# Performance work log

Hardware: AMD Instinct MI355X
Metric: run time of the kernel (lower is better)

## Reference

```python
import jax, jax.numpy as jnp
import numpy as np

K = 3          # k_neighbors
EPS = 1e-12    # F.normalize eps


def _l2norm(x):
    n = jnp.sqrt(jnp.sum(x * x, axis=-1, keepdims=True))
    return x / jnp.maximum(n, EPS)


def setup_inputs() -> dict:
    key = jax.random.key(0)
    k1, k2 = jax.random.split(key)
    query_features = jax.random.normal(k1, (64, 64, 32, 32), dtype=jnp.float32)
    support_features = jax.random.normal(k2, (64, 5, 64, 1024), dtype=jnp.float32)
    return {"query_features": query_features, "support_features": support_features}


def reference(query_features, support_features):
    B, D, h, w = query_features.shape
    # (B, Nq, D), L2-normalized along D
    q_local = _l2norm(query_features.reshape(B, D, h * w).transpose(0, 2, 1))
    # support: (B, Way, D, Ns) -> (B, Way, Ns, D), L2-normalized along D
    s_local = _l2norm(support_features.transpose(0, 1, 3, 2))
    # cosine similarities for all (batch, way) pairs in one batched matmul
    sim = jnp.einsum('bqd,bwsd->bwqs', q_local, s_local)  # (B, Way, Nq, Ns)
    k_actual = min(K, sim.shape[-1])
    topk_sim, _ = jax.lax.top_k(sim, k_actual)            # (B, Way, Nq, k)
    return topk_sim.sum(axis=(-1, -2))                    # (B, Way)
```

## Files before the change

kernel.cpp:

```cpp
#include <hip/hip_runtime.h>
#include <hip/hip_bf16.h>


using bf16x8 = __attribute__((ext_vector_type(8))) short;
using f32x4  = __attribute__((ext_vector_type(4))) float;

__device__ inline unsigned cvt_pk_bf16(float lo, float hi) {
    unsigned r;
    asm("v_cvt_pk_bf16_f32 %0, %1, %2" : "=v"(r) : "v"(lo), "v"(hi));
    return r;
}

__device__ inline uint4 pack8cvt(const float* v) {
    uint4 r;
    r.x = cvt_pk_bf16(v[0], v[1]);
    r.y = cvt_pk_bf16(v[2], v[3]);
    r.z = cvt_pk_bf16(v[4], v[5]);
    r.w = cvt_pk_bf16(v[6], v[7]);
    return r;
}

#define INS(v, T0, T1, T2) do {                         \
    float _v = (v);                                     \
    float _n0 = fmaxf((T0), _v);                        \
    float _n1 = __builtin_amdgcn_fmed3f(_v, (T0), (T1));\
    float _n2 = __builtin_amdgcn_fmed3f(_v, (T1), (T2));\
    (T0) = _n0; (T1) = _n1; (T2) = _n2;                 \
} while (0)


__global__ __launch_bounds__(256) void prep_all(const float* __restrict__ Q,
                                                const float* __restrict__ S,
                                                uint4* __restrict__ Qbf,
                                                uint4* __restrict__ Sbf,
                                                float* __restrict__ rnq) {
    const int blk = blockIdx.x;
    if (blk < 256) {
        const int b = blk >> 2;
        const int col = ((blk & 3) << 8) + threadIdx.x;
        const float* p = Q + (size_t)b * 65536 + col;
        float v[64];
        #pragma unroll
        for (int d = 0; d < 64; ++d) v[d] = p[(size_t)d << 10];
        float ss = 0.f;
        #pragma unroll
        for (int d = 0; d < 64; ++d) ss += v[d] * v[d];
        rnq[(b << 10) + col] = 1.0f / fmaxf(sqrtf(ss), 1e-12f);
        uint4* ob = Qbf + ((size_t)(b << 6) + (col >> 4)) * 128 + (col & 15);
        #pragma unroll
        for (int h = 0; h < 8; ++h)
            ob[h << 4] = pack8cvt(&v[h << 3]);
    } else {
        const int bw = (blk - 256) >> 2;
        const int col = ((blk & 3) << 8) + threadIdx.x;
        const float* p = S + (size_t)bw * 65536 + col;
        float v[64];
        #pragma unroll
        for (int d = 0; d < 64; ++d) v[d] = p[(size_t)d << 10];
        float ss = 0.f;
        #pragma unroll
        for (int d = 0; d < 64; ++d) ss += v[d] * v[d];
        const float rs = 1.0f / fmaxf(sqrtf(ss), 1e-12f);
        #pragma unroll
        for (int d = 0; d < 64; ++d) v[d] *= rs;
        uint4* ob = Sbf + ((size_t)(bw << 6) + (col >> 4)) * 128 + (col & 15);
        #pragma unroll
        for (int h = 0; h < 8; ++h)
            ob[h << 4] = pack8cvt(&v[h << 3]);
    }
}

__global__ __launch_bounds__(256) void knn_main(const uint4* __restrict__ Qbf,
                                                const uint4* __restrict__ Sbf,
                                                const float* __restrict__ rnq,
                                                float* __restrict__ partial) {
    __shared__ float wsum[4];
    const int lin = blockIdx.x;
    const int l   = (lin & 7) * 160 + (lin >> 3);
    const int qc  = l & 3;
    const int bw  = l >> 2;
    const int b   = bw / 5;
    const int wv = threadIdx.x >> 6, lane = threadIdx.x & 63;

    const uint4* qb = Qbf + ((size_t)(b << 6) + (qc << 4) + (wv << 2)) * 128 + lane;
    bf16x8 bq[4][2];
    #pragma unroll
    for (int qt = 0; qt < 4; ++qt)
        #pragma unroll
        for (int c = 0; c < 2; ++c)
            bq[qt][c] = *reinterpret_cast<const bf16x8*>(&qb[qt * 128 + (c << 6)]);

    const uint4* sb = Sbf + (size_t)(bw << 6) * 128 + lane;

    float t0[4], t1[4], t2[4];
    #pragma unroll
    for (int qt = 0; qt < 4; ++qt) { t0[qt] = -1e30f; t1[qt] = -1e30f; t2[qt] = -1e30f; }

    bf16x8 abuf[4][2];
    #pragma unroll
    for (int i = 0; i < 3; ++i) {
        abuf[i][0] = *reinterpret_cast<const bf16x8*>(&sb[i * 128]);
        abuf[i][1] = *reinterpret_cast<const bf16x8*>(&sb[i * 128 + 64]);
    }
    #pragma unroll 4
    for (int st = 0; st < 64; ++st) {
        if (st + 3 < 64) {
            abuf[(st + 3) & 3][0] = *reinterpret_cast<const bf16x8*>(&sb[(st + 3) * 128]);
            abuf[(st + 3) & 3][1] = *reinterpret_cast<const bf16x8*>(&sb[(st + 3) * 128 + 64]);
        }
        #pragma unroll
        for (int qt = 0; qt < 4; ++qt) {
            f32x4 c = {0.f, 0.f, 0.f, 0.f};
            c = __builtin_amdgcn_mfma_f32_16x16x32_bf16(abuf[st & 3][0], bq[qt][0], c, 0, 0, 0);
            c = __builtin_amdgcn_mfma_f32_16x16x32_bf16(abuf[st & 3][1], bq[qt][1], c, 0, 0, 0);
            #pragma unroll
            for (int j = 0; j < 4; ++j)
                INS(c[j], t0[qt], t1[qt], t2[qt]);
        }
    }

    float s3 = 0.f;
    #pragma unroll
    for (int qt = 0; qt < 4; ++qt) {
        #pragma unroll
        for (int m = 16; m <= 32; m <<= 1) {
            float b0 = __shfl_xor(t0[qt], m);
            float b1 = __shfl_xor(t1[qt], m);
            float b2 = __shfl_xor(t2[qt], m);
            INS(b0, t0[qt], t1[qt], t2[qt]);
            INS(b1, t0[qt], t1[qt], t2[qt]);
            INS(b2, t0[qt], t1[qt], t2[qt]);
        }
        const int qg = (qc << 8) + (wv << 6) + (qt << 4) + (lane & 15);
        s3 += (t0[qt] + t1[qt] + t2[qt]) * rnq[(b << 10) + qg];
    }
    #pragma unroll
    for (int m = 1; m < 64; m <<= 1) s3 += __shfl_xor(s3, m);
    s3 *= 0.25f;
    if (lane == 0) wsum[wv] = s3;
    __syncthreads();
    if (threadIdx.x == 0)
        partial[((size_t)bw << 2) + qc] = (wsum[0] + wsum[1]) + (wsum[2] + wsum[3]);
}

__global__ void finalize4(const float* __restrict__ partial, float* __restrict__ out) {
    int i = blockIdx.x * blockDim.x + threadIdx.x;
    if (i < 320)
        out[i] = (partial[4 * i] + partial[4 * i + 1]) +
                 (partial[4 * i + 2] + partial[4 * i + 3]);
}

__global__ void norms_kernel(const float* __restrict__ Q, const float* __restrict__ S,
                             float* __restrict__ rnq, float* __restrict__ rns) {
    int gid = blockIdx.x * blockDim.x + threadIdx.x;
    if (gid < 65536) {
        int b = gid >> 10, qi = gid & 1023;
        const float* p = Q + (size_t)b * 65536 + qi;
        float ss = 0.f;
        #pragma unroll
        for (int d = 0; d < 64; ++d) { float v = p[(size_t)d * 1024]; ss += v * v; }
        rnq[gid] = 1.0f / fmaxf(sqrtf(ss), 1e-12f);
    } else {
        int v = gid - 65536;
        int bw = v >> 10, si = v & 1023;
        const float* p = S + (size_t)bw * 65536 + si;
        float ss = 0.f;
        #pragma unroll
        for (int d = 0; d < 64; ++d) { float x = p[(size_t)d * 1024]; ss += x * x; }
        rns[v] = 1.0f / fmaxf(sqrtf(ss), 1e-12f);
    }
}

__global__ __launch_bounds__(512, 4) void knn_fb(
        const float* __restrict__ Q, const float* __restrict__ S,
        const float* __restrict__ rnq, const float* __restrict__ rns,
        float* __restrict__ partial) {
    __shared__ uint4 qfrag[16 * 128];
    __shared__ uint4 sfrag[2][4 * 128];
    __shared__ float wsum[8];

    const int qc = blockIdx.x, w = blockIdx.y, b = blockIdx.z;
    const int t = threadIdx.x, wv = t >> 6, lane = t & 63;

    const float* Qb   = Q + (size_t)b * 65536;
    const float* Sb   = S + (size_t)(b * 5 + w) * 65536;
    const float* rnqb = rnq + (b << 10);
    const float* rnsb = rns + ((b * 5 + w) << 10);

    bf16x8 bq[4][2];
    for (int ph = 0; ph < 2; ++ph) {
        for (int sub = 0; sub < 4; ++sub) {
            int qg = (qc << 9) + (ph << 8) + (sub << 6) + lane;
            float v[8];
            #pragma unroll
            for (int i = 0; i < 8; ++i)
                v[i] = Qb[(size_t)((wv << 3) + i) * 1024 + qg];
            qfrag[((sub << 2) + (lane >> 4)) * 128 + (wv << 4) + (lane & 15)] = pack8cvt(v);
        }
        __syncthreads();
        if ((wv >> 2) == ph) {
            #pragma unroll
            for (int qt = 0; qt < 4; ++qt)
                #pragma unroll
                for (int c = 0; c < 2; ++c)
                    bq[qt][c] = *reinterpret_cast<const bf16x8*>(
                        &qfrag[(((wv & 3) << 2) + qt) * 128 + (c << 6) + lane]);
        }
        __syncthreads();
    }

    {
        float sv[8]; float rs = rnsb[lane];
        #pragma unroll
        for (int i = 0; i < 8; ++i)
            sv[i] = Sb[(size_t)((wv << 3) + i) * 1024 + lane] * rs;
        sfrag[0][(lane >> 4) * 128 + (wv << 4) + (lane & 15)] = pack8cvt(sv);
    }
    __syncthreads();

    float t0[4], t1[4], t2[4];
    #pragma unroll
    for (int qt = 0; qt < 4; ++qt) { t0[qt] = -1e30f; t1[qt] = -1e30f; t2[qt] = -1e30f; }
    int cur = 0;
    const float* sp = Sb + ((wv << 3) << 10) + lane;

    for (int blk = 0; blk < 16; ++blk) {
        float sv[8]; float rs;
        if (blk < 15) {
            const int sb_ = (blk + 1) << 6;
            rs = rnsb[sb_ + lane];
            #pragma unroll
            for (int i = 0; i < 8; ++i)
                sv[i] = sp[(size_t)(i << 10) + sb_];
        }
        #pragma unroll
        for (int st = 0; st < 4; ++st) {
            bf16x8 a0 = *reinterpret_cast<const bf16x8*>(&sfrag[cur][st * 128 + lane]);
            bf16x8 a1 = *reinterpret_cast<const bf16x8*>(&sfrag[cur][st * 128 + 64 + lane]);
            #pragma unroll
            for (int qt = 0; qt < 4; ++qt) {
                f32x4 c = {0.f, 0.f, 0.f, 0.f};
                c = __builtin_amdgcn_mfma_f32_16x16x32_bf16(a0, bq[qt][0], c, 0, 0, 0);
                c = __builtin_amdgcn_mfma_f32_16x16x32_bf16(a1, bq[qt][1], c, 0, 0, 0);
                #pragma unroll
                for (int j = 0; j < 4; ++j)
                    INS(c[j], t0[qt], t1[qt], t2[qt]);
            }
        }
        if (blk < 15) {
            #pragma unroll
            for (int i = 0; i < 8; ++i) sv[i] *= rs;
            sfrag[cur ^ 1][(lane >> 4) * 128 + (wv << 4) + (lane & 15)] = pack8cvt(sv);
        }
        __syncthreads();
        cur ^= 1;
    }

    float s3 = 0.f;
    #pragma unroll
    for (int qt = 0; qt < 4; ++qt) {
        #pragma unroll
        for (int m = 16; m <= 32; m <<= 1) {
            float b0 = __shfl_xor(t0[qt], m);
            float b1 = __shfl_xor(t1[qt], m);
            float b2 = __shfl_xor(t2[qt], m);
            INS(b0, t0[qt], t1[qt], t2[qt]);
            INS(b1, t0[qt], t1[qt], t2[qt]);
            INS(b2, t0[qt], t1[qt], t2[qt]);
        }
        int qg = (qc << 9) + (wv << 6) + (qt << 4) + (lane & 15);
        s3 += (t0[qt] + t1[qt] + t2[qt]) * rnqb[qg];
    }
    #pragma unroll
    for (int m = 1; m < 64; m <<= 1) s3 += __shfl_xor(s3, m);
    s3 *= 0.25f;
    if (lane == 0) wsum[wv] = s3;
    __syncthreads();
    if (t == 0) {
        float acc = 0.f;
        #pragma unroll
        for (int i = 0; i < 8; ++i) acc += wsum[i];
        partial[((b * 5 + w) << 1) + qc] = acc;
    }
}

__global__ void finalize2(const float* __restrict__ partial, float* __restrict__ out) {
    int i = blockIdx.x * blockDim.x + threadIdx.x;
    if (i < 320)
        out[i] = partial[2 * i] + partial[2 * i + 1];
}

extern "C" void kernel_launch(void* const* d_in, const int* in_sizes, int n_in,
                              void* d_out, int out_size, void* d_ws, size_t ws_size,
                              hipStream_t stream) {
    const float* Q = (const float*)d_in[0];
    const float* S = (const float*)d_in[1];
    float* out = (float*)d_out;

    const size_t NEED = 8388608ull + 41943040ull + 262144ull + 5120ull;
    if (ws_size >= NEED) {
        uint4* Qbf    = (uint4*)d_ws;
        uint4* Sbf    = (uint4*)((char*)d_ws + 8388608ull);
        float* rnq    = (float*)((char*)d_ws + 8388608ull + 41943040ull);
        float* partial= (float*)((char*)d_ws + 8388608ull + 41943040ull + 262144ull);
        prep_all<<<1536, 256, 0, stream>>>(Q, S, Qbf, Sbf, rnq);
        knn_main<<<1280, 256, 0, stream>>>(Qbf, Sbf, rnq, partial);
        finalize4<<<2, 256, 0, stream>>>(partial, out);
    } else {
        float* rnq = (float*)d_ws;
        float* rns = rnq + 65536;
        float* partial = rns + 327680;
        norms_kernel<<<(65536 + 327680) / 256, 256, 0, stream>>>(Q, S, rnq, rns);
        knn_fb<<<dim3(2, 5, 64), 512, 0, stream>>>(Q, S, rnq, rns, partial);
        finalize2<<<2, 256, 0, stream>>>(partial, out);
    }
}
```

Measured before the change: 96.50 us.

## Split support columns across two blocks and merge per-query top-3 in separate kernel

Each knn_main block now scans half of the support set, doubling the grid to 2560 blocks, and writes its per-query top-3 values to three workspace arrays. A new knn_merge kernel combines the two halves' top-3, applies the query norm scaling, and reduces to the final per-(batch,way) output, replacing finalize4. This is meant to raise parallelism and occupancy in the main kernel, at the cost of extra global traffic for the partial top-k arrays, a larger workspace requirement, and a heavier merge kernel.

```diff
diff --git a/kernel.cpp b/kernel.cpp
--- a/kernel.cpp
+++ b/kernel.cpp
@@ -72,14 +72,15 @@
 
 __global__ __launch_bounds__(256) void knn_main(const uint4* __restrict__ Qbf,
                                                 const uint4* __restrict__ Sbf,
-                                                const float* __restrict__ rnq,
-                                                float* __restrict__ partial) {
-    __shared__ float wsum[4];
-    const int lin = blockIdx.x;
-    const int l   = (lin & 7) * 160 + (lin >> 3);
-    const int qc  = l & 3;
-    const int bw  = l >> 2;
-    const int b   = bw / 5;
+                                                float* __restrict__ P0,
+                                                float* __restrict__ P1,
+                                                float* __restrict__ P2) {
+    const int lin  = blockIdx.x;
+    const int l    = (lin & 7) * 320 + (lin >> 3);
+    const int half = l & 1;
+    const int qc   = (l >> 1) & 3;
+    const int bw   = l >> 3;
+    const int b    = bw / 5;
     const int wv = threadIdx.x >> 6, lane = threadIdx.x & 63;
 
     const uint4* qb = Qbf + ((size_t)(b << 6) + (qc << 4) + (wv << 2)) * 128 + lane;
@@ -90,7 +91,7 @@
         for (int c = 0; c < 2; ++c)
             bq[qt][c] = *reinterpret_cast<const bf16x8*>(&qb[qt * 128 + (c << 6)]);
 
-    const uint4* sb = Sbf + (size_t)(bw << 6) * 128 + lane;
+    const uint4* sb = Sbf + ((size_t)(bw << 6) + (half << 5)) * 128 + lane;
 
     float t0[4], t1[4], t2[4];
     #pragma unroll
@@ -103,8 +104,8 @@
         abuf[i][1] = *reinterpret_cast<const bf16x8*>(&sb[i * 128 + 64]);
     }
     #pragma unroll 4
-    for (int st = 0; st < 64; ++st) {
-        if (st + 3 < 64) {
+    for (int st = 0; st < 32; ++st) {
+        if (st + 3 < 32) {
             abuf[(st + 3) & 3][0] = *reinterpret_cast<const bf16x8*>(&sb[(st + 3) * 128]);
             abuf[(st + 3) & 3][1] = *reinterpret_cast<const bf16x8*>(&sb[(st + 3) * 128 + 64]);
         }
@@ -119,7 +120,6 @@
         }
     }
 
-    float s3 = 0.f;
     #pragma unroll
     for (int qt = 0; qt < 4; ++qt) {
         #pragma unroll
@@ -131,23 +131,46 @@
             INS(b1, t0[qt], t1[qt], t2[qt]);
             INS(b2, t0[qt], t1[qt], t2[qt]);
         }
-        const int qg = (qc << 8) + (wv << 6) + (qt << 4) + (lane & 15);
-        s3 += (t0[qt] + t1[qt] + t2[qt]) * rnq[(b << 10) + qg];
-    }
-    #pragma unroll
-    for (int m = 1; m < 64; m <<= 1) s3 += __shfl_xor(s3, m);
-    s3 *= 0.25f;
-    if (lane == 0) wsum[wv] = s3;
+    }
+    if (lane < 16) {
+        const size_t e0 = (size_t)bw * 2048 + (half << 10) + (qc << 8) + (wv << 6) + lane;
+        #pragma unroll
+        for (int qt = 0; qt < 4; ++qt) {
+            P0[e0 + (qt << 4)] = t0[qt];
+            P1[e0 + (qt << 4)] = t1[qt];
+            P2[e0 + (qt << 4)] = t2[qt];
+        }
+    }
+}
+
+__global__ __launch_bounds__(1024) void knn_merge(const float* __restrict__ P0,
+                                                  const float* __restrict__ P1,
+                                                  const float* __restrict__ P2,
+                                                  const float* __restrict__ rnq,
+                                                  float* __restrict__ out) {
+    __shared__ float wsum[16];
+    const int bw = blockIdx.x;
+    const int q  = threadIdx.x;
+    const int b  = bw / 5;
+    const size_t e = (size_t)bw * 2048 + q;
+
+    float t0 = P0[e], t1 = P1[e], t2 = P2[e];
+    float u0 = P0[e + 1024], u1 = P1[e + 1024], u2 = P2[e + 1024];
+    INS(u0, t0, t1, t2);
+    INS(u1, t0, t1, t2);
+    INS(u2, t0, t1, t2);
+    float s = (t0 + t1 + t2) * rnq[(b << 10) + q];
+
+    #pragma unroll
+    for (int m = 1; m < 64; m <<= 1) s += __shfl_xor(s, m);
+    if ((q & 63) == 0) wsum[q >> 6] = s;
     __syncthreads();
-    if (threadIdx.x == 0)
-        partial[((size_t)bw << 2) + qc] = (wsum[0] + wsum[1]) + (wsum[2] + wsum[3]);
-}
-
-__global__ void finalize4(const float* __restrict__ partial, float* __restrict__ out) {
-    int i = blockIdx.x * blockDim.x + threadIdx.x;
-    if (i < 320)
-        out[i] = (partial[4 * i] + partial[4 * i + 1]) +
-                 (partial[4 * i + 2] + partial[4 * i + 3]);
+    if (q < 16) {
+        float v = wsum[q];
+        #pragma unroll
+        for (int m = 1; m < 16; m <<= 1) v += __shfl_xor(v, m);
+        if (q == 0) out[bw] = v;
+    }
 }
 
 __global__ void norms_kernel(const float* __restrict__ Q, const float* __restrict__ S,
@@ -297,15 +320,19 @@
     const float* S = (const float*)d_in[1];
     float* out = (float*)d_out;
 
-    const size_t NEED = 8388608ull + 41943040ull + 262144ull + 5120ull;
+    const size_t QBF = 8388608ull, SBF = 41943040ull, RNQ = 262144ull, PL = 2621440ull;
+    const size_t NEED = QBF + SBF + RNQ + 3 * PL;
     if (ws_size >= NEED) {
-        uint4* Qbf    = (uint4*)d_ws;
-        uint4* Sbf    = (uint4*)((char*)d_ws + 8388608ull);
-        float* rnq    = (float*)((char*)d_ws + 8388608ull + 41943040ull);
-        float* partial= (float*)((char*)d_ws + 8388608ull + 41943040ull + 262144ull);
+        char* base = (char*)d_ws;
+        uint4* Qbf = (uint4*)base;
+        uint4* Sbf = (uint4*)(base + QBF);
+        float* rnq = (float*)(base + QBF + SBF);
+        float* P0  = (float*)(base + QBF + SBF + RNQ);
+        float* P1  = (float*)(base + QBF + SBF + RNQ + PL);
+        float* P2  = (float*)(base + QBF + SBF + RNQ + 2 * PL);
         prep_all<<<1536, 256, 0, stream>>>(Q, S, Qbf, Sbf, rnq);
-        knn_main<<<1280, 256, 0, stream>>>(Qbf, Sbf, rnq, partial);
-        finalize4<<<2, 256, 0, stream>>>(partial, out);
+        knn_main<<<2560, 256, 0, stream>>>(Qbf, Sbf, P0, P1, P2);
+        knn_merge<<<320, 1024, 0, stream>>>(P0, P1, P2, rnq, out);
     } else {
         float* rnq = (float*)d_ws;
         float* rns = rnq + 65536;
```

After: 99.20 us. +2.8%, slower.

## Stream support tiles through an LDS ring via direct global-to-LDS loads

Applied to the files above, without the earlier changes.

Replaces the per-wave register prefetch of the support tiles in knn_main with a block-shared 8-slot LDS ring filled by global_load_lds, four tiles in flight, with vmcnt waits and barriers between stages. Each wave now loads only a quarter of each tile, so the block shares the loads instead of every wave fetching the same support data separately. This cuts redundant global traffic and frees the registers used by the old prefetch buffer, but adds two barriers per iteration and uses 32KB of LDS per block, which may limit occupancy.

```diff
diff --git a/kernel.cpp b/kernel.cpp
--- a/kernel.cpp
+++ b/kernel.cpp
@@ -27,6 +27,13 @@
     float _n2 = __builtin_amdgcn_fmed3f(_v, (T1), (T2));\
     (T0) = _n0; (T1) = _n1; (T2) = _n2;                 \
 } while (0)
+
+__device__ inline void gload16(const void* g, void* lds) {
+    __builtin_amdgcn_global_load_lds(
+        (const __attribute__((address_space(1))) unsigned int*)g,
+        (__attribute__((address_space(3))) unsigned int*)lds,
+        16, 0, 0);
+}
 
 
 __global__ __launch_bounds__(256) void prep_all(const float* __restrict__ Q,
@@ -74,6 +81,7 @@
                                                 const uint4* __restrict__ Sbf,
                                                 const float* __restrict__ rnq,
                                                 float* __restrict__ partial) {
+    __shared__ uint4 ring[8 * 256];
     __shared__ float wsum[4];
     const int lin = blockIdx.x;
     const int l   = (lin & 7) * 160 + (lin >> 3);
@@ -90,153 +98,27 @@
         for (int c = 0; c < 2; ++c)
             bq[qt][c] = *reinterpret_cast<const bf16x8*>(&qb[qt * 128 + (c << 6)]);
 
-    const uint4* sb = Sbf + (size_t)(bw << 6) * 128 + lane;
+    const char* sbase = (const char*)(Sbf + (size_t)(bw << 6) * 128);
+    const size_t toff = (size_t)threadIdx.x * 16;
 
     float t0[4], t1[4], t2[4];
     #pragma unroll
     for (int qt = 0; qt < 4; ++qt) { t0[qt] = -1e30f; t1[qt] = -1e30f; t2[qt] = -1e30f; }
 
-    bf16x8 abuf[4][2];
-    #pragma unroll
-    for (int i = 0; i < 3; ++i) {
-        abuf[i][0] = *reinterpret_cast<const bf16x8*>(&sb[i * 128]);
-        abuf[i][1] = *reinterpret_cast<const bf16x8*>(&sb[i * 128 + 64]);
-    }
-    #pragma unroll 4
-    for (int st = 0; st < 64; ++st) {
-        if (st + 3 < 64) {
-            abuf[(st + 3) & 3][0] = *reinterpret_cast<const bf16x8*>(&sb[(st + 3) * 128]);
-            abuf[(st + 3) & 3][1] = *reinterpret_cast<const bf16x8*>(&sb[(st + 3) * 128 + 64]);
-        }
-        #pragma unroll
-        for (int qt = 0; qt < 4; ++qt) {
-            f32x4 c = {0.f, 0.f, 0.f, 0.f};
-            c = __builtin_amdgcn_mfma_f32_16x16x32_bf16(abuf[st & 3][0], bq[qt][0], c, 0, 0, 0);
-            c = __builtin_amdgcn_mfma_f32_16x16x32_bf16(abuf[st & 3][1], bq[qt][1], c, 0, 0, 0);
-            #pragma unroll
-            for (int j = 0; j < 4; ++j)
-                INS(c[j], t0[qt], t1[qt], t2[qt]);
-        }
-    }
-
-    float s3 = 0.f;
-    #pragma unroll
-    for (int qt = 0; qt < 4; ++qt) {
-        #pragma unroll
-        for (int m = 16; m <= 32; m <<= 1) {
-            float b0 = __shfl_xor(t0[qt], m);
-            float b1 = __shfl_xor(t1[qt], m);
-            float b2 = __shfl_xor(t2[qt], m);
-            INS(b0, t0[qt], t1[qt], t2[qt]);
-            INS(b1, t0[qt], t1[qt], t2[qt]);
-            INS(b2, t0[qt], t1[qt], t2[qt]);
-        }
-        const int qg = (qc << 8) + (wv << 6) + (qt << 4) + (lane & 15);
-        s3 += (t0[qt] + t1[qt] + t2[qt]) * rnq[(b << 10) + qg];
-    }
-    #pragma unroll
-    for (int m = 1; m < 64; m <<= 1) s3 += __shfl_xor(s3, m);
-    s3 *= 0.25f;
-    if (lane == 0) wsum[wv] = s3;
-    __syncthreads();
-    if (threadIdx.x == 0)
-        partial[((size_t)bw << 2) + qc] = (wsum[0] + wsum[1]) + (wsum[2] + wsum[3]);
-}
-
-__global__ void finalize4(const float* __restrict__ partial, float* __restrict__ out) {
-    int i = blockIdx.x * blockDim.x + threadIdx.x;
-    if (i < 320)
-        out[i] = (partial[4 * i] + partial[4 * i + 1]) +
-                 (partial[4 * i + 2] + partial[4 * i + 3]);
-}
-
-__global__ void norms_kernel(const float* __restrict__ Q, const float* __restrict__ S,
-                             float* __restrict__ rnq, float* __restrict__ rns) {
-    int gid = blockIdx.x * blockDim.x + threadIdx.x;
-    if (gid < 65536) {
-        int b = gid >> 10, qi = gid & 1023;
-        const float* p = Q + (size_t)b * 65536 + qi;
-        float ss = 0.f;
-        #pragma unroll
-        for (int d = 0; d < 64; ++d) { float v = p[(size_t)d * 1024]; ss += v * v; }
-        rnq[gid] = 1.0f / fmaxf(sqrtf(ss), 1e-12f);
-    } else {
-        int v = gid - 65536;
-        int bw = v >> 10, si = v & 1023;
-        const float* p = S + (size_t)bw * 65536 + si;
-        float ss = 0.f;
-        #pragma unroll
-        for (int d = 0; d < 64; ++d) { float x = p[(size_t)d * 1024]; ss += x * x; }
-        rns[v] = 1.0f / fmaxf(sqrtf(ss), 1e-12f);
-    }
-}
-
-__global__ __launch_bounds__(512, 4) void knn_fb(
-        const float* __restrict__ Q, const float* __restrict__ S,
-        const float* __restrict__ rnq, const float* __restrict__ rns,
-        float* __restrict__ partial) {
-    __shared__ uint4 qfrag[16 * 128];
-    __shared__ uint4 sfrag[2][4 * 128];
-    __shared__ float wsum[8];
-
-    const int qc = blockIdx.x, w = blockIdx.y, b = blockIdx.z;
-    const int t = threadIdx.x, wv = t >> 6, lane = t & 63;
-
-    const float* Qb   = Q + (size_t)b * 65536;
-    const float* Sb   = S + (size_t)(b * 5 + w) * 65536;
-    const float* rnqb = rnq + (b << 10);
-    const float* rnsb = rns + ((b * 5 + w) << 10);
-
-    bf16x8 bq[4][2];
-    for (int ph = 0; ph < 2; ++ph) {
-        for (int sub = 0; sub < 4; ++sub) {
-            int qg = (qc << 9) + (ph << 8) + (sub << 6) + lane;
-            float v[8];
-            #pragma unroll
-            for (int i = 0; i < 8; ++i)
-                v[i] = Qb[(size_t)((wv << 3) + i) * 1024 + qg];
-            qfrag[((sub << 2) + (lane >> 4)) * 128 + (wv << 4) + (lane & 15)] = pack8cvt(v);
-        }
-        __syncthreads();
-        if ((wv >> 2) == ph) {
-            #pragma unroll
-            for (int qt = 0; qt < 4; ++qt)
-                #pragma unroll
-                for (int c = 0; c < 2; ++c)
-                    bq[qt][c] = *reinterpret_cast<const bf16x8*>(
-                        &qfrag[(((wv & 3) << 2) + qt) * 128 + (c << 6) + lane]);
-        }
-        __syncthreads();
-    }
-
-    {
-        float sv[8]; float rs = rnsb[lane];
-        #pragma unroll
-        for (int i = 0; i < 8; ++i)
-            sv[i] = Sb[(size_t)((wv << 3) + i) * 1024 + lane] * rs;
-        sfrag[0][(lane >> 4) * 128 + (wv << 4) + (lane & 15)] = pack8cvt(sv);
-    }
-    __syncthreads();
-
-    float t0[4], t1[4], t2[4];
-    #pragma unroll
-    for (int qt = 0; qt < 4; ++qt) { t0[qt] = -1e30f; t1[qt] = -1e30f; t2[qt] = -1e30f; }
-    int cur = 0;
-    const float* sp = Sb + ((wv << 3) << 10) + lane;
-
-    for (int blk = 0; blk < 16; ++blk) {
-        float sv[8]; float rs;
-        if (blk < 15) {
-            const int sb_ = (blk + 1) << 6;
-            rs = rnsb[sb_ + lane];
-            #pragma unroll
-            for (int i = 0; i < 8; ++i)
-                sv[i] = sp[(size_t)(i << 10) + sb_];
-        }
-        #pragma unroll
-        for (int st = 0; st < 4; ++st) {
-            bf16x8 a0 = *reinterpret_cast<const bf16x8*>(&sfrag[cur][st * 128 + lane]);
-            bf16x8 a1 = *reinterpret_cast<const bf16x8*>(&sfrag[cur][st * 128 + 64 + lane]);
+    #pragma unroll
+    for (int p = 0; p < 4; ++p)
+        gload16(sbase + (size_t)p * 4096 + toff, &ring[(p << 8) + (wv << 6)]);
+
+    for (int p = 0; p < 28; ++p) {
+        gload16(sbase + (size_t)(p + 4) * 4096 + toff,
+                &ring[(((p + 4) & 7) << 8) + (wv << 6)]);
+        asm volatile("s_waitcnt vmcnt(4)" ::: "memory");
+        __builtin_amdgcn_s_barrier();
+        const uint4* sp = &ring[((p & 7) << 8)];
+        #pragma unroll
+        for (int tt = 0; tt < 2; ++tt) {
+            bf16x8 a0 = *reinterpret_cast<const bf16x8*>(&sp[tt * 128 + lane]);
+            bf16x8 a1 = *reinterpret_cast<const bf16x8*>(&sp[tt * 128 + 64 + lane]);
             #pragma unroll
             for (int qt = 0; qt < 4; ++qt) {
                 f32x4 c = {0.f, 0.f, 0.f, 0.f};
@@ -247,13 +129,26 @@
                     INS(c[j], t0[qt], t1[qt], t2[qt]);
             }
         }
-        if (blk < 15) {
-            #pragma unroll
-            for (int i = 0; i < 8; ++i) sv[i] *= rs;
-            sfrag[cur ^ 1][(lane >> 4) * 128 + (wv << 4) + (lane & 15)] = pack8cvt(sv);
-        }
-        __syncthreads();
-        cur ^= 1;
+        __builtin_amdgcn_s_barrier();
+    }
+    asm volatile("s_waitcnt vmcnt(0)" ::: "memory");
+    __builtin_amdgcn_s_barrier();
+    for (int p = 28; p < 32; ++p) {
+        const uint4* sp = &ring[((p & 7) << 8)];
+        #pragma unroll
+        for (int tt = 0; tt < 2; ++tt) {
+            bf16x8 a0 = *reinterpret_cast<const bf16x8*>(&sp[tt * 128 + lane]);
+            bf16x8 a1 = *reinterpret_cast<const bf16x8*>(&sp[tt * 128 + 64 + lane]);
+            #pragma unroll
+            for (int qt = 0; qt < 4; ++qt) {
+                f32x4 c = {0.f, 0.f, 0.f, 0.f};
+                c = __builtin_amdgcn_mfma_f32_16x16x32_bf16(a0, bq[qt][0], c, 0, 0, 0);
+                c = __builtin_amdgcn_mfma_f32_16x16x32_bf16(a1, bq[qt][1], c, 0, 0, 0);
+                #pragma unroll
+                for (int j = 0; j < 4; ++j)
+                    INS(c[j], t0[qt], t1[qt], t2[qt]);
+            }
+        }
     }
 
     float s3 = 0.f;
@@ -268,6 +163,143 @@
             INS(b1, t0[qt], t1[qt], t2[qt]);
             INS(b2, t0[qt], t1[qt], t2[qt]);
         }
+        const int qg = (qc << 8) + (wv << 6) + (qt << 4) + (lane & 15);
+        s3 += (t0[qt] + t1[qt] + t2[qt]) * rnq[(b << 10) + qg];
+    }
+    #pragma unroll
+    for (int m = 1; m < 64; m <<= 1) s3 += __shfl_xor(s3, m);
+    s3 *= 0.25f;
+    if (lane == 0) wsum[wv] = s3;
+    __syncthreads();
+    if (threadIdx.x == 0)
+        partial[((size_t)bw << 2) + qc] = (wsum[0] + wsum[1]) + (wsum[2] + wsum[3]);
+}
+
+__global__ void finalize4(const float* __restrict__ partial, float* __restrict__ out) {
+    int i = blockIdx.x * blockDim.x + threadIdx.x;
+    if (i < 320)
+        out[i] = (partial[4 * i] + partial[4 * i + 1]) +
+                 (partial[4 * i + 2] + partial[4 * i + 3]);
+}
+
+__global__ void norms_kernel(const float* __restrict__ Q, const float* __restrict__ S,
+                             float* __restrict__ rnq, float* __restrict__ rns) {
+    int gid = blockIdx.x * blockDim.x + threadIdx.x;
+    if (gid < 65536) {
+        int b = gid >> 10, qi = gid & 1023;
+        const float* p = Q + (size_t)b * 65536 + qi;
+        float ss = 0.f;
+        #pragma unroll
+        for (int d = 0; d < 64; ++d) { float v = p[(size_t)d * 1024]; ss += v * v; }
+        rnq[gid] = 1.0f / fmaxf(sqrtf(ss), 1e-12f);
+    } else {
+        int v = gid - 65536;
+        int bw = v >> 10, si = v & 1023;
+        const float* p = S + (size_t)bw * 65536 + si;
+        float ss = 0.f;
+        #pragma unroll
+        for (int d = 0; d < 64; ++d) { float x = p[(size_t)d * 1024]; ss += x * x; }
+        rns[v] = 1.0f / fmaxf(sqrtf(ss), 1e-12f);
+    }
+}
+
+__global__ __launch_bounds__(512, 4) void knn_fb(
+        const float* __restrict__ Q, const float* __restrict__ S,
+        const float* __restrict__ rnq, const float* __restrict__ rns,
+        float* __restrict__ partial) {
+    __shared__ uint4 qfrag[16 * 128];
+    __shared__ uint4 sfrag[2][4 * 128];
+    __shared__ float wsum[8];
+
+    const int qc = blockIdx.x, w = blockIdx.y, b = blockIdx.z;
+    const int t = threadIdx.x, wv = t >> 6, lane = t & 63;
+
+    const float* Qb   = Q + (size_t)b * 65536;
+    const float* Sb   = S + (size_t)(b * 5 + w) * 65536;
+    const float* rnqb = rnq + (b << 10);
+    const float* rnsb = rns + ((b * 5 + w) << 10);
+
+    bf16x8 bq[4][2];
+    for (int ph = 0; ph < 2; ++ph) {
+        for (int sub = 0; sub < 4; ++sub) {
+            int qg = (qc << 9) + (ph << 8) + (sub << 6) + lane;
+            float v[8];
+            #pragma unroll
+            for (int i = 0; i < 8; ++i)
+                v[i] = Qb[(size_t)((wv << 3) + i) * 1024 + qg];
+            qfrag[((sub << 2) + (lane >> 4)) * 128 + (wv << 4) + (lane & 15)] = pack8cvt(v);
+        }
+        __syncthreads();
+        if ((wv >> 2) == ph) {
+            #pragma unroll
+            for (int qt = 0; qt < 4; ++qt)
+                #pragma unroll
+                for (int c = 0; c < 2; ++c)
+                    bq[qt][c] = *reinterpret_cast<const bf16x8*>(
+                        &qfrag[(((wv & 3) << 2) + qt) * 128 + (c << 6) + lane]);
+        }
+        __syncthreads();
+    }
+
+    {
+        float sv[8]; float rs = rnsb[lane];
+        #pragma unroll
+        for (int i = 0; i < 8; ++i)
+            sv[i] = Sb[(size_t)((wv << 3) + i) * 1024 + lane] * rs;
+        sfrag[0][(lane >> 4) * 128 + (wv << 4) + (lane & 15)] = pack8cvt(sv);
+    }
+    __syncthreads();
+
+    float t0[4], t1[4], t2[4];
+    #pragma unroll
+    for (int qt = 0; qt < 4; ++qt) { t0[qt] = -1e30f; t1[qt] = -1e30f; t2[qt] = -1e30f; }
+    int cur = 0;
+    const float* sp = Sb + ((wv << 3) << 10) + lane;
+
+    for (int blk = 0; blk < 16; ++blk) {
+        float sv[8]; float rs;
+        if (blk < 15) {
+            const int sb_ = (blk + 1) << 6;
+            rs = rnsb[sb_ + lane];
+            #pragma unroll
+            for (int i = 0; i < 8; ++i)
+                sv[i] = sp[(size_t)(i << 10) + sb_];
+        }
+        #pragma unroll
+        for (int st = 0; st < 4; ++st) {
+            bf16x8 a0 = *reinterpret_cast<const bf16x8*>(&sfrag[cur][st * 128 + lane]);
+            bf16x8 a1 = *reinterpret_cast<const bf16x8*>(&sfrag[cur][st * 128 + 64 + lane]);
+            #pragma unroll
+            for (int qt = 0; qt < 4; ++qt) {
+                f32x4 c = {0.f, 0.f, 0.f, 0.f};
+                c = __builtin_amdgcn_mfma_f32_16x16x32_bf16(a0, bq[qt][0], c, 0, 0, 0);
+                c = __builtin_amdgcn_mfma_f32_16x16x32_bf16(a1, bq[qt][1], c, 0, 0, 0);
+                #pragma unroll
+                for (int j = 0; j < 4; ++j)
+                    INS(c[j], t0[qt], t1[qt], t2[qt]);
+            }
+        }
+        if (blk < 15) {
+            #pragma unroll
+            for (int i = 0; i < 8; ++i) sv[i] *= rs;
+            sfrag[cur ^ 1][(lane >> 4) * 128 + (wv << 4) + (lane & 15)] = pack8cvt(sv);
+        }
+        __syncthreads();
+        cur ^= 1;
+    }
+
+    float s3 = 0.f;
+    #pragma unroll
+    for (int qt = 0; qt < 4; ++qt) {
+        #pragma unroll
+        for (int m = 16; m <= 32; m <<= 1) {
+            float b0 = __shfl_xor(t0[qt], m);
+            float b1 = __shfl_xor(t1[qt], m);
+            float b2 = __shfl_xor(t2[qt], m);
+            INS(b0, t0[qt], t1[qt], t2[qt]);
+            INS(b1, t0[qt], t1[qt], t2[qt]);
+            INS(b2, t0[qt], t1[qt], t2[qt]);
+        }
         int qg = (qc << 9) + (wv << 6) + (qt << 4) + (lane & 15);
         s3 += (t0[qt] + t1[qt] + t2[qt]) * rnqb[qg];
     }
@@ -297,12 +329,14 @@
     const float* S = (const float*)d_in[1];
     float* out = (float*)d_out;
 
-    const size_t NEED = 8388608ull + 41943040ull + 262144ull + 5120ull;
+    const size_t QBF = 8388608ull, SBF = 41943040ull, RNQ = 262144ull;
+    const size_t NEED = QBF + SBF + RNQ + 5120ull;
     if (ws_size >= NEED) {
-        uint4* Qbf    = (uint4*)d_ws;
-        uint4* Sbf    = (uint4*)((char*)d_ws + 8388608ull);
-        float* rnq    = (float*)((char*)d_ws + 8388608ull + 41943040ull);
-        float* partial= (float*)((char*)d_ws + 8388608ull + 41943040ull + 262144ull);
+        char* base = (char*)d_ws;
+        uint4* Qbf     = (uint4*)base;
+        uint4* Sbf     = (uint4*)(base + QBF);
+        float* rnq     = (float*)(base + QBF + SBF);
+        float* partial = (float*)(base + QBF + SBF + RNQ);
         prep_all<<<1536, 256, 0, stream>>>(Q, S, Qbf, Sbf, rnq);
         knn_main<<<1280, 256, 0, stream>>>(Qbf, Sbf, rnq, partial);
         finalize4<<<2, 256, 0, stream>>>(partial, out);
```

After: 101.2 us. +4.9%, slower.
